# Kernel optimization log

Measured on AMD Instinct MI355X. Metric: run time of the kernel, lower is better.

## Reference

```python
import jax, jax.numpy as jnp
import numpy as np
from jax import lax

B, L, D = 8, 2048, 512


def _mlp(x, w1, w2):
    # MemoryMLP: x + gelu(x @ w1) @ w2  (exact gelu, matching F.gelu default)
    return x + jax.nn.gelu(x @ w1, approximate=False) @ w2


def _l2norm(t):
    # F.normalize(p=2, dim=-1, eps=1e-12)
    n = jnp.linalg.norm(t, axis=-1, keepdims=True)
    return t / jnp.maximum(n, 1e-12)


def setup_inputs() -> dict:
    key = jax.random.key(0)
    ks = jax.random.split(key, 12)
    s = 0.02
    return {
        "x": jax.random.normal(ks[0], (B, L, D), jnp.float32),
        "conv_w": jax.random.normal(ks[1], (D, 1, 4), jnp.float32) * s,  # depthwise, (out, in/groups, k)
        "conv_b": jax.random.normal(ks[2], (D,), jnp.float32) * s,
        "q_w": jax.random.normal(ks[3], (D, D), jnp.float32) * s,  # Linear weight (out, in)
        "mem_w1": jax.random.normal(ks[4], (D, D), jnp.float32) * s,
        "mem_w2": jax.random.normal(ks[5], (D, D), jnp.float32) * s,
        "eta_w1": jax.random.normal(ks[6], (D, D), jnp.float32) * s,
        "eta_w2": jax.random.normal(ks[7], (D, D), jnp.float32) * s,
        "alpha_w1": jax.random.normal(ks[8], (D, D), jnp.float32) * s,
        "alpha_w2": jax.random.normal(ks[9], (D, D), jnp.float32) * s,
    }


def _forward(x, conv_w, conv_b, q_w, mem_w1, mem_w2, eta_w1, eta_w2, alpha_w1, alpha_w2):
    # causal depthwise conv: Conv1d(k=4, padding=3, groups=D) then slice [:L] == left-pad 3
    xc = lax.conv_general_dilated(
        jnp.transpose(x, (0, 2, 1)),  # (B, D, L)
        conv_w,                        # (D, 1, 4)
        window_strides=(1,),
        padding=[(3, 0)],
        feature_group_count=D,
        dimension_numbers=("NCH", "OIH", "NCH"),
    ) + conv_b[None, :, None]
    xc = jnp.transpose(xc, (0, 2, 1))  # (B, L, D)

    # time-invariant branches (m_k/m_v weights are never updated; kt/vt/hat_v do not
    # affect the output, so they are elided). q, eta, alpha use fixed weights -> vectorize.
    q = _l2norm(xc @ q_w.T)                                   # (B, L, D)
    eta_mean = jax.nn.sigmoid(_mlp(xc, eta_w1, eta_w2)).mean(axis=(0, 2))      # (L,)
    alpha_mean = jax.nn.sigmoid(_mlp(xc, alpha_w1, alpha_w2)).mean(axis=(0, 2))  # (L,)

    def step(carry, inp):
        w1, w2 = carry
        q_t, a_t, e_t = inp  # (B, D), (), ()
        o_t = _mlp(q_t, w1, w2)  # output uses pre-update memory
        new_w1 = w1 * a_t - e_t * 0.01
        new_w2 = w2 * a_t - e_t * 0.01
        return (new_w1, new_w2), o_t

    qs = jnp.transpose(q, (1, 0, 2))  # (L, B, D)
    (_, _), outs = lax.scan(step, (mem_w1, mem_w2), (qs, alpha_mean, eta_mean))
    return jnp.transpose(outs, (1, 0, 2))  # (B, L, D)


def reference(x, conv_w, conv_b, q_w, mem_w1, mem_w2, eta_w1, eta_w2, alpha_w1, alpha_w2):
    return _forward(x, conv_w, conv_b, q_w, mem_w1, mem_w2, eta_w1, eta_w2, alpha_w1, alpha_w2)
```

## Files before the change

### kernel.cpp

```cpp
#include <hip/hip_runtime.h>
#include <math.h>

constexpr int Bn = 8, Ln = 2048, Dn = 512;
constexpr int Mn = Bn * Ln;
constexpr int CONV_BLOCKS = Mn * Dn / 16 / 256;
constexpr int WPREP_BLOCKS = 448;
constexpr int ZERO_FLOATS = 3 * Mn + 2 * Ln;
constexpr int ZERO_BLOCKS = ZERO_FLOATS / (256 * 4);

typedef __bf16 bf16x8 __attribute__((ext_vector_type(8)));
typedef __bf16 bf16x4v __attribute__((ext_vector_type(4)));
typedef float f32x4 __attribute__((ext_vector_type(4)));

__device__ __forceinline__ float gelu_exact(float x) {
    return 0.5f * x * (1.0f + erff(x * 0.7071067811865475f));
}
__device__ __forceinline__ float sigmoid_fast(float x) {
    return __builtin_amdgcn_rcpf(1.0f + __expf(-x));
}

__global__ __launch_bounds__(256) void prep_kernel(
    const float* __restrict__ x, const float* __restrict__ w,
    const float* __restrict__ bias, __bf16* __restrict__ xcb,
    const float* __restrict__ ew1, const float* __restrict__ aw1,
    const float* __restrict__ ew2, const float* __restrict__ aw2,
    const float* __restrict__ mw1, const float* __restrict__ mw2,
    const float* __restrict__ qw,
    __bf16* __restrict__ Wall, __bf16* __restrict__ W2t,
    __bf16* __restrict__ m1t, __bf16* __restrict__ m2t,
    float* __restrict__ zero_zone) {
    __shared__ float tile[64][65];
    if (blockIdx.x < CONV_BLOCKS) {
        int idx = blockIdx.x * 256 + threadIdx.x;
        int g = idx & 127;
        int r4 = idx >> 7;
        int bl0 = r4 * 4;
        int l0 = bl0 & (Ln - 1);
        int d = g * 4;
        float4 b4 = *(const float4*)&bias[d];
        float wv[16];
        *(float4*)&wv[0]  = *(const float4*)&w[d * 4];
        *(float4*)&wv[4]  = *(const float4*)&w[d * 4 + 4];
        *(float4*)&wv[8]  = *(const float4*)&w[d * 4 + 8];
        *(float4*)&wv[12] = *(const float4*)&w[d * 4 + 12];
        float4 xv[7];
#pragma unroll
        for (int t = 0; t < 7; ++t) {
            int ll = l0 - 3 + t;
            xv[t] = (ll >= 0 && t < 7) ? *(const float4*)&x[(size_t)(bl0 - 3 + t) * Dn + d]
                                       : make_float4(0.f, 0.f, 0.f, 0.f);
            if (t >= 3) {
                if (l0 - 3 + t < Ln) xv[t] = *(const float4*)&x[(size_t)(bl0 - 3 + t) * Dn + d];
            }
        }
#pragma unroll
        for (int i = 0; i < 4; ++i) {
            float a0 = b4.x, a1 = b4.y, a2 = b4.z, a3 = b4.w;
#pragma unroll
            for (int k = 0; k < 4; ++k) {
                float4 xt = xv[i + k];
                a0 += xt.x * wv[0 * 4 + k];
                a1 += xt.y * wv[1 * 4 + k];
                a2 += xt.z * wv[2 * 4 + k];
                a3 += xt.w * wv[3 * 4 + k];
            }
            bf16x4v o = { (__bf16)a0, (__bf16)a1, (__bf16)a2, (__bf16)a3 };
            *(bf16x4v*)&xcb[(size_t)(bl0 + i) * Dn + d] = o;
        }
        return;
    }
    if (blockIdx.x >= CONV_BLOCKS + WPREP_BLOCKS) {
        int idx = (blockIdx.x - CONV_BLOCKS - WPREP_BLOCKS) * 256 + threadIdx.x;
        ((float4*)zero_zone)[idx] = make_float4(0.f, 0.f, 0.f, 0.f);
        return;
    }
    int bid = blockIdx.x - CONV_BLOCKS;
    int z = bid >> 6;
    int t = bid & 63;
    int r0 = (t >> 3) * 64, c0 = (t & 7) * 64;
    const float* src;
    __bf16* dst;
    int trans = 1;
    switch (z) {
        case 0: src = ew1; dst = Wall; break;
        case 1: src = aw1; dst = Wall + 512 * 512; break;
        case 2: src = ew2; dst = W2t; break;
        case 3: src = aw2; dst = W2t + 512 * 512; break;
        case 4: src = mw1; dst = m1t; break;
        case 5: src = mw2; dst = m2t; break;
        default: src = qw; dst = Wall + 1024 * 512; trans = 0; break;
    }
    if (!trans) {
        for (int i = threadIdx.x; i < 4096; i += 256) {
            int r = i >> 6, c = i & 63;
            dst[(size_t)(r0 + r) * 512 + c0 + c] = (__bf16)src[(size_t)(r0 + r) * 512 + c0 + c];
        }
        return;
    }
    for (int i = threadIdx.x; i < 4096; i += 256) {
        int r = i >> 6, c = i & 63;
        tile[r][c] = src[(size_t)(r0 + r) * 512 + c0 + c];
    }
    __syncthreads();
    for (int i = threadIdx.x; i < 4096; i += 256) {
        int r = i >> 6, c = i & 63;
        dst[(size_t)(c0 + r) * 512 + r0 + c] = (__bf16)tile[c][r];
    }
}

template <int OP, int BM>
__global__ __launch_bounds__(256, 4) void gemm_mfma(
    const __bf16* __restrict__ A, int lda, int Az,
    const __bf16* __restrict__ Bt, int Bz,
    void* __restrict__ C0, void* __restrict__ C1,
    const __bf16* __restrict__ auxb,
    const float* __restrict__ Pv, const float* __restrict__ Qv,
    const float* __restrict__ SSv, const float* __restrict__ RSv,
    float* __restrict__ red0, float* __restrict__ red1, float* __restrict__ red2) {
    constexpr int MI = BM / 32;
    constexpr int AISS = BM / 64;
    __shared__ __align__(16) __bf16 Asl[BM * 32];
    __shared__ __align__(16) __bf16 Bsl[128 * 32];
    const int tid = threadIdx.x;
    const int lane = tid & 63, wv = tid >> 6;
    const int wm = wv & 1, wn = wv >> 1;
    const int fr = lane & 15, fq = lane >> 4;
    const int z = blockIdx.z;
    A += (size_t)z * Az;
    Bt += (size_t)z * Bz;
    const __bf16* Ab = A + (size_t)blockIdx.y * BM * lda;
    const __bf16* Bb = Bt + (size_t)blockIdx.x * 128 * 512;
    float* redp = (OP == 1) ? red0 + (size_t)z * Ln : red0;

    f32x4 acc[MI][4] = {};

    for (int k0 = 0; k0 < 512; k0 += 32) {
#pragma unroll
        for (int i = 0; i < AISS; ++i) {
            int c = tid + i * 256;
            int r = c >> 2, co = (c & 3) * 8;
            __builtin_amdgcn_global_load_lds(
                (const __attribute__((address_space(1))) void*)(Ab + (size_t)r * lda + k0 + co),
                (__attribute__((address_space(3))) void*)(Asl + c * 8), 16, 0, 0);
        }
#pragma unroll
        for (int i = 0; i < 2; ++i) {
            int c = tid + i * 256;
            int r = c >> 2, co = (c & 3) * 8;
            __builtin_amdgcn_global_load_lds(
                (const __attribute__((address_space(1))) void*)(Bb + (size_t)r * 512 + k0 + co),
                (__attribute__((address_space(3))) void*)(Bsl + c * 8), 16, 0, 0);
        }
        __syncthreads();
        bf16x8 af[MI], bfr[4];
#pragma unroll
        for (int mi = 0; mi < MI; ++mi)
            af[mi] = *(const bf16x8*)&Asl[(wm * (BM / 2) + mi * 16 + fr) * 32 + fq * 8];
#pragma unroll
        for (int ni = 0; ni < 4; ++ni)
            bfr[ni] = *(const bf16x8*)&Bsl[(wn * 64 + ni * 16 + fr) * 32 + fq * 8];
#pragma unroll
        for (int mi = 0; mi < MI; ++mi)
#pragma unroll
            for (int ni = 0; ni < 4; ++ni)
                acc[mi][ni] = __builtin_amdgcn_mfma_f32_16x16x32_bf16(af[mi], bfr[ni], acc[mi][ni], 0, 0, 0);
        __syncthreads();
    }

    const int row_base = blockIdx.y * BM + wm * (BM / 2);
    const int col_base = blockIdx.x * 128 + wn * 64;
    const bool qpath = (OP == 0) && (blockIdx.x >= 8);
#pragma unroll
    for (int mi = 0; mi < MI; ++mi) {
#pragma unroll
        for (int r = 0; r < 4; ++r) {
            int row = row_base + mi * 16 + fq * 4 + r;
            float p = 0.f, qs = 0.f, rs = 0.f, inv = 1.f;
            if (OP >= 3) {
                int t = row & (Ln - 1);
                p = Pv[t]; qs = Qv[t];
                rs = RSv[row];
                inv = 1.0f / fmaxf(sqrtf(SSv[row]), 1e-12f);
            }
            float s1 = 0.f, s2 = 0.f;
#pragma unroll
            for (int ni = 0; ni < 4; ++ni) {
                int col = col_base + ni * 16 + fr;
                float v = acc[mi][ni][r];
                if (OP == 0) {
                    if (!qpath) {
                        v = gelu_exact(v);
                        ((__bf16*)C0)[(size_t)row * 1024 + col] = (__bf16)v;
                    } else {
                        ((__bf16*)C1)[(size_t)row * 512 + col - 1024] = (__bf16)v;
                        s1 += v; s2 += v * v;
                    }
                } else if (OP == 1) {
                    v = sigmoid_fast((float)auxb[(size_t)row * 512 + col] + v);
                    s1 += v;
                } else if (OP == 3) {
                    v = gelu_exact(inv * (p * v + qs * rs));
                    ((__bf16*)C0)[(size_t)row * 512 + col] = (__bf16)v;
                    s1 += v;
                } else if (OP == 4) {
                    float qn = (float)auxb[(size_t)row * 512 + col] * inv;
                    ((float*)C0)[(size_t)row * 512 + col] = qn + p * v + qs * rs;
                }
            }
            if (OP == 1 || OP == 3 || (OP == 0 && qpath)) {
                s1 += __shfl_xor(s1, 1, 64);
                s1 += __shfl_xor(s1, 2, 64);
                s1 += __shfl_xor(s1, 4, 64);
                s1 += __shfl_xor(s1, 8, 64);
                if (OP == 0) {
                    s2 += __shfl_xor(s2, 1, 64);
                    s2 += __shfl_xor(s2, 2, 64);
                    s2 += __shfl_xor(s2, 4, 64);
                    s2 += __shfl_xor(s2, 8, 64);
                }
                if (fr == 0) {
                    if (OP == 1) atomicAdd(&redp[row & (Ln - 1)], s1 * (1.0f / 4096.0f));
                    else if (OP == 3) atomicAdd(&red0[row], s1);
                    else { atomicAdd(&red1[row], s2); atomicAdd(&red2[row], s1); }
                }
            }
        }
    }
}

__global__ __launch_bounds__(256) void scan_kernel(const float* __restrict__ a,
                                                   const float* __restrict__ e,
                                                   float* __restrict__ P,
                                                   float* __restrict__ Q) {
    int tid = threadIdx.x;
    int base = tid * 8;
    float la[8], le[8], Aloc[8], Bloc[8];
#pragma unroll
    for (int j = 0; j < 8; ++j) { la[j] = a[base + j]; le[j] = e[base + j]; }
    float Ac = 1.f, Bc = 0.f;
#pragma unroll
    for (int j = 0; j < 8; ++j) {
        Aloc[j] = Ac; Bloc[j] = Bc;
        Bc = Bc * la[j] - 0.01f * le[j];
        Ac *= la[j];
    }
    float Aw = Ac, Bw = Bc;
#pragma unroll
    for (int off = 1; off < 64; off <<= 1) {
        float Ap = __shfl_up(Aw, off, 64);
        float Bp = __shfl_up(Bw, off, 64);
        if ((tid & 63) >= off) { Bw = Aw * Bp + Bw; Aw = Aw * Ap; }
    }
    __shared__ float wA[4], wB[4];
    if ((tid & 63) == 63) { wA[tid >> 6] = Aw; wB[tid >> 6] = Bw; }
    __syncthreads();
    float Apre = 1.f, Bpre = 0.f;
    for (int w = 0; w < (tid >> 6); ++w) { Bpre = wA[w] * Bpre + wB[w]; Apre = wA[w] * Apre; }
    float Ax = __shfl_up(Aw, 1, 64), Bx = __shfl_up(Bw, 1, 64);
    if ((tid & 63) == 0) { Ax = 1.f; Bx = 0.f; }
    float At = Ax * Apre, Bt2 = Ax * Bpre + Bx;
#pragma unroll
    for (int j = 0; j < 8; ++j) {
        P[base + j] = Aloc[j] * At;
        Q[base + j] = Aloc[j] * Bt2 + Bloc[j];
    }
}

extern "C" void kernel_launch(void* const* d_in, const int* in_sizes, int n_in,
                              void* d_out, int out_size, void* d_ws, size_t ws_size,
                              hipStream_t stream) {
    const float* x        = (const float*)d_in[0];
    const float* conv_w   = (const float*)d_in[1];
    const float* conv_b   = (const float*)d_in[2];
    const float* q_w      = (const float*)d_in[3];
    const float* mem_w1   = (const float*)d_in[4];
    const float* mem_w2   = (const float*)d_in[5];
    const float* eta_w1   = (const float*)d_in[6];
    const float* eta_w2   = (const float*)d_in[7];
    const float* alpha_w1 = (const float*)d_in[8];
    const float* alpha_w2 = (const float*)d_in[9];
    float* out = (float*)d_out;

    char* w = (char*)d_ws;
    __bf16* xcb  = (__bf16*)w;    w += (size_t)Mn * Dn * 2;
    __bf16* H    = (__bf16*)w;    w += (size_t)Mn * 1024 * 2;
    __bf16* qb   = (__bf16*)w;    w += (size_t)Mn * Dn * 2;
    __bf16* G    = (__bf16*)w;    w += (size_t)Mn * Dn * 2;
    __bf16* Wall = (__bf16*)w;    w += (size_t)1536 * 512 * 2;
    __bf16* W2t  = (__bf16*)w;    w += (size_t)2 * 512 * 512 * 2;
    __bf16* m1t  = (__bf16*)w;    w += (size_t)512 * 512 * 2;
    __bf16* m2t  = (__bf16*)w;    w += (size_t)512 * 512 * 2;
    float* Rv      = (float*)w;   w += (size_t)Mn * 4;
    float* MeanAcc = (float*)w;   w += (size_t)2 * Ln * 4;
    float* SS      = (float*)w;   w += (size_t)Mn * 4;
    float* RS      = (float*)w;   w += (size_t)Mn * 4;
    float* Pv = (float*)w;        w += Ln * 4;
    float* Qv = (float*)w;        w += Ln * 4;

    prep_kernel<<<CONV_BLOCKS + WPREP_BLOCKS + ZERO_BLOCKS, 256, 0, stream>>>(
        x, conv_w, conv_b, xcb, eta_w1, alpha_w1, eta_w2, alpha_w2,
        mem_w1, mem_w2, q_w, Wall, W2t, m1t, m2t, Rv);
    gemm_mfma<0, 128><<<dim3(12, 128), 256, 0, stream>>>(
        xcb, 512, 0, Wall, 0, H, qb, nullptr,
        nullptr, nullptr, nullptr, nullptr, nullptr, SS, RS);
    gemm_mfma<1, 128><<<dim3(4, 128, 2), 256, 0, stream>>>(
        H, 1024, 512, W2t, 512 * 512, nullptr, nullptr, xcb,
        nullptr, nullptr, nullptr, nullptr, MeanAcc, nullptr, nullptr);
    scan_kernel<<<1, 256, 0, stream>>>(MeanAcc + Ln, MeanAcc, Pv, Qv);
    gemm_mfma<3, 64><<<dim3(4, 256), 256, 0, stream>>>(
        qb, 512, 0, m1t, 0, G, nullptr, nullptr,
        Pv, Qv, SS, RS, Rv, nullptr, nullptr);
    gemm_mfma<4, 64><<<dim3(4, 256), 256, 0, stream>>>(
        G, 512, 0, m2t, 0, out, nullptr, qb,
        Pv, Qv, SS, Rv, nullptr, nullptr, nullptr);
}
```

Measured before the change: 245.6 us.

## Replace LDS-staged GEMM with register-prefetched direct global MFMA loads

Rewrites the bf16 MFMA GEMM so each wave loads its A and B fragments straight from global memory into registers, double-buffered across k steps, removing LDS staging and both block barriers per k-iteration. All four GEMM launches now use 128-row tiles (the last two previously used 64), and launch bounds drop to 3 waves per SIMD to make room for the larger register footprint. It also simplifies the conv halo load logic. The risk is uncoalesced 16-byte global loads with no data sharing between waves through LDS, which increases L2 traffic and may stall on latency.

Measured after the change: 388.4 us. 58.1% more time.

```diff
diff --git a/kernel.cpp b/kernel.cpp
--- a/kernel.cpp
+++ b/kernel.cpp
@@ -47,11 +47,8 @@
 #pragma unroll
         for (int t = 0; t < 7; ++t) {
             int ll = l0 - 3 + t;
-            xv[t] = (ll >= 0 && t < 7) ? *(const float4*)&x[(size_t)(bl0 - 3 + t) * Dn + d]
-                                       : make_float4(0.f, 0.f, 0.f, 0.f);
-            if (t >= 3) {
-                if (l0 - 3 + t < Ln) xv[t] = *(const float4*)&x[(size_t)(bl0 - 3 + t) * Dn + d];
-            }
+            xv[t] = (ll >= 0) ? *(const float4*)&x[(size_t)(bl0 - 3 + t) * Dn + d]
+                              : make_float4(0.f, 0.f, 0.f, 0.f);
         }
 #pragma unroll
         for (int i = 0; i < 4; ++i) {
@@ -108,8 +105,8 @@
     }
 }
 
-template <int OP, int BM>
-__global__ __launch_bounds__(256, 4) void gemm_mfma(
+template <int OP>
+__global__ __launch_bounds__(256, 3) void gemm_reg(
     const __bf16* __restrict__ A, int lda, int Az,
     const __bf16* __restrict__ Bt, int Bz,
     void* __restrict__ C0, void* __restrict__ C1,
@@ -117,10 +114,6 @@
     const float* __restrict__ Pv, const float* __restrict__ Qv,
     const float* __restrict__ SSv, const float* __restrict__ RSv,
     float* __restrict__ red0, float* __restrict__ red1, float* __restrict__ red2) {
-    constexpr int MI = BM / 32;
-    constexpr int AISS = BM / 64;
-    __shared__ __align__(16) __bf16 Asl[BM * 32];
-    __shared__ __align__(16) __bf16 Bsl[128 * 32];
     const int tid = threadIdx.x;
     const int lane = tid & 63, wv = tid >> 6;
     const int wm = wv & 1, wn = wv >> 1;
@@ -128,53 +121,43 @@
     const int z = blockIdx.z;
     A += (size_t)z * Az;
     Bt += (size_t)z * Bz;
-    const __bf16* Ab = A + (size_t)blockIdx.y * BM * lda;
-    const __bf16* Bb = Bt + (size_t)blockIdx.x * 128 * 512;
+    const int row0 = blockIdx.y * 128 + wm * 64;
+    const int col0 = blockIdx.x * 128 + wn * 64;
+    const __bf16* Ap = A + (size_t)(row0 + fr) * lda + fq * 8;
+    const __bf16* Bp = Bt + (size_t)(col0 + fr) * 512 + fq * 8;
     float* redp = (OP == 1) ? red0 + (size_t)z * Ln : red0;
 
-    f32x4 acc[MI][4] = {};
-
+    f32x4 acc[4][4] = {};
+    bf16x8 ab[2][4], bb[2][4];
+#pragma unroll
+    for (int s = 0; s < 4; ++s) {
+        ab[0][s] = *(const bf16x8*)(Ap + (size_t)s * 16 * lda);
+        bb[0][s] = *(const bf16x8*)(Bp + s * 16 * 512);
+    }
+#pragma unroll
     for (int k0 = 0; k0 < 512; k0 += 32) {
-#pragma unroll
-        for (int i = 0; i < AISS; ++i) {
-            int c = tid + i * 256;
-            int r = c >> 2, co = (c & 3) * 8;
-            __builtin_amdgcn_global_load_lds(
-                (const __attribute__((address_space(1))) void*)(Ab + (size_t)r * lda + k0 + co),
-                (__attribute__((address_space(3))) void*)(Asl + c * 8), 16, 0, 0);
-        }
-#pragma unroll
-        for (int i = 0; i < 2; ++i) {
-            int c = tid + i * 256;
-            int r = c >> 2, co = (c & 3) * 8;
-            __builtin_amdgcn_global_load_lds(
-                (const __attribute__((address_space(1))) void*)(Bb + (size_t)r * 512 + k0 + co),
-                (__attribute__((address_space(3))) void*)(Bsl + c * 8), 16, 0, 0);
-        }
-        __syncthreads();
-        bf16x8 af[MI], bfr[4];
-#pragma unroll
-        for (int mi = 0; mi < MI; ++mi)
-            af[mi] = *(const bf16x8*)&Asl[(wm * (BM / 2) + mi * 16 + fr) * 32 + fq * 8];
-#pragma unroll
-        for (int ni = 0; ni < 4; ++ni)
-            bfr[ni] = *(const bf16x8*)&Bsl[(wn * 64 + ni * 16 + fr) * 32 + fq * 8];
-#pragma unroll
-        for (int mi = 0; mi < MI; ++mi)
+        const int cur = (k0 >> 5) & 1, nxt = cur ^ 1;
+        if (k0 < 480) {
+#pragma unroll
+            for (int s = 0; s < 4; ++s) {
+                ab[nxt][s] = *(const bf16x8*)(Ap + (size_t)s * 16 * lda + k0 + 32);
+                bb[nxt][s] = *(const bf16x8*)(Bp + s * 16 * 512 + k0 + 32);
+            }
+        }
+#pragma unroll
+        for (int mi = 0; mi < 4; ++mi)
 #pragma unroll
             for (int ni = 0; ni < 4; ++ni)
-                acc[mi][ni] = __builtin_amdgcn_mfma_f32_16x16x32_bf16(af[mi], bfr[ni], acc[mi][ni], 0, 0, 0);
-        __syncthreads();
-    }
-
-    const int row_base = blockIdx.y * BM + wm * (BM / 2);
-    const int col_base = blockIdx.x * 128 + wn * 64;
+                acc[mi][ni] = __builtin_amdgcn_mfma_f32_16x16x32_bf16(
+                    ab[cur][mi], bb[cur][ni], acc[mi][ni], 0, 0, 0);
+    }
+
     const bool qpath = (OP == 0) && (blockIdx.x >= 8);
 #pragma unroll
-    for (int mi = 0; mi < MI; ++mi) {
+    for (int mi = 0; mi < 4; ++mi) {
 #pragma unroll
         for (int r = 0; r < 4; ++r) {
-            int row = row_base + mi * 16 + fq * 4 + r;
+            int row = row0 + mi * 16 + fq * 4 + r;
             float p = 0.f, qs = 0.f, rs = 0.f, inv = 1.f;
             if (OP >= 3) {
                 int t = row & (Ln - 1);
@@ -185,7 +168,7 @@
             float s1 = 0.f, s2 = 0.f;
 #pragma unroll
             for (int ni = 0; ni < 4; ++ni) {
-                int col = col_base + ni * 16 + fr;
+                int col = col0 + ni * 16 + fr;
                 float v = acc[mi][ni][r];
                 if (OP == 0) {
                     if (!qpath) {
@@ -300,17 +283,17 @@
     prep_kernel<<<CONV_BLOCKS + WPREP_BLOCKS + ZERO_BLOCKS, 256, 0, stream>>>(
         x, conv_w, conv_b, xcb, eta_w1, alpha_w1, eta_w2, alpha_w2,
         mem_w1, mem_w2, q_w, Wall, W2t, m1t, m2t, Rv);
-    gemm_mfma<0, 128><<<dim3(12, 128), 256, 0, stream>>>(
+    gemm_reg<0><<<dim3(12, 128), 256, 0, stream>>>(
         xcb, 512, 0, Wall, 0, H, qb, nullptr,
         nullptr, nullptr, nullptr, nullptr, nullptr, SS, RS);
-    gemm_mfma<1, 128><<<dim3(4, 128, 2), 256, 0, stream>>>(
+    gemm_reg<1><<<dim3(4, 128, 2), 256, 0, stream>>>(
         H, 1024, 512, W2t, 512 * 512, nullptr, nullptr, xcb,
         nullptr, nullptr, nullptr, nullptr, MeanAcc, nullptr, nullptr);
     scan_kernel<<<1, 256, 0, stream>>>(MeanAcc + Ln, MeanAcc, Pv, Qv);
-    gemm_mfma<3, 64><<<dim3(4, 256), 256, 0, stream>>>(
+    gemm_reg<3><<<dim3(4, 128), 256, 0, stream>>>(
         qb, 512, 0, m1t, 0, G, nullptr, nullptr,
         Pv, Qv, SS, RS, Rv, nullptr, nullptr);
-    gemm_mfma<4, 64><<<dim3(4, 256), 256, 0, stream>>>(
+    gemm_reg<4><<<dim3(4, 128), 256, 0, stream>>>(
         G, 512, 0, m2t, 0, out, nullptr, qb,
         Pv, Qv, SS, Rv, nullptr, nullptr, nullptr);
 }
```
